# Optimization experiments

Hardware: AMD Instinct MI355X
Metric: run time of the kernel (lower is better)

## Reference

```python
import jax, jax.numpy as jnp
import numpy as np

NB, NX, NU, NY, NQ = 8192, 512, 128, 128, 256


def setup_inputs() -> dict:
    key = jax.random.key(0)
    ks = jax.random.split(key, 13)
    x = jax.random.normal(ks[0], (NB, NX), dtype=jnp.float32)
    u = jax.random.normal(ks[1], (NB, NU), dtype=jnp.float32)
    C1 = jax.random.normal(ks[2], (NQ, NX), dtype=jnp.float32) / np.sqrt(NX).astype(np.float32)
    D11 = jax.random.normal(ks[3], (NQ, NQ), dtype=jnp.float32) / np.sqrt(NQ).astype(np.float32)
    D12 = jax.random.normal(ks[4], (NQ, NU), dtype=jnp.float32) / np.sqrt(NU).astype(np.float32)
    # Lambda is a positive-diagonal matrix (only Lambda[k,k] is used in the recurrence)
    lam_diag = jax.random.uniform(ks[5], (NQ,), dtype=jnp.float32, minval=0.5, maxval=1.5)
    Lambda = jnp.diag(lam_diag)
    bv = 0.1 * jax.random.normal(ks[6], (NQ, 1), dtype=jnp.float32)
    # E must be invertible (set by the REN wrapper in the original code)
    E = jnp.eye(NX, dtype=jnp.float32) + 0.05 * jax.random.normal(ks[7], (NX, NX), dtype=jnp.float32) / np.sqrt(NX).astype(np.float32)
    F = jax.random.normal(ks[8], (NX, NX), dtype=jnp.float32) / np.sqrt(NX).astype(np.float32)
    B1 = jax.random.normal(ks[9], (NX, NQ), dtype=jnp.float32) / np.sqrt(NQ).astype(np.float32)
    B2 = jax.random.normal(ks[10], (NX, NU), dtype=jnp.float32) / np.sqrt(NU).astype(np.float32)
    C2 = jax.random.normal(ks[11], (NY, NX), dtype=jnp.float32) / np.sqrt(NX).astype(np.float32)
    D21 = jax.random.normal(ks[12], (NY, NQ), dtype=jnp.float32) / np.sqrt(NQ).astype(np.float32)
    return {"x": x, "u": u, "C1": C1, "D11": D11, "D12": D12, "Lambda": Lambda,
            "bv": bv, "E": E, "F": F, "B1": B1, "B2": B2, "C2": C2, "D21": D21}


def _solve_w(x, u, C1, D11, D12, lam_diag, bv):
    # Loop-invariant part of v_k: x @ C1[k]^T + u @ D12[k]^T + bv[k]
    base = x @ C1.T + u @ D12.T + bv[:, 0][None, :]  # (nb, nq)
    nb = x.shape[0]
    nq = C1.shape[0]

    def step(w, k):
        # w columns >= k are still zero, matching the torch loop semantics
        v = (base[:, k] + w @ D11[k]) / lam_diag[k]  # (nb,)
        w = w.at[:, k].set(jnp.tanh(v))
        return w, None

    w0 = jnp.zeros((nb, nq), dtype=x.dtype)
    w, _ = jax.lax.scan(step, w0, jnp.arange(nq))
    return w


def reference(x, u, C1, D11, D12, Lambda, bv, E, F, B1, B2, C2, D21):
    lam_diag = jnp.diagonal(Lambda)
    w = _solve_w(x, u, C1, D11, D12, lam_diag, bv)
    # E^{-1} @ M computed via solve (same math as torch.inverse(E) @ M)
    EinvF = jnp.linalg.solve(E, F)
    EinvB1 = jnp.linalg.solve(E, B1)
    EinvB2 = jnp.linalg.solve(E, B2)
    dx = x @ EinvF.T + w @ EinvB1.T + u @ EinvB2.T
    y = x @ C2.T + w @ D21.T
    return (dx, y)
```

## Files before the change

### kernel.cpp

```cpp
#include <hip/hip_runtime.h>

typedef unsigned short u16;
typedef unsigned int   u32;
typedef __attribute__((ext_vector_type(8))) __bf16 bf16x8;
typedef __attribute__((ext_vector_type(4))) float  f32x4;
typedef __attribute__((ext_vector_type(4))) u16    u16x4;
typedef __attribute__((ext_vector_type(4))) u32    u32x4;

#define DEV __device__ __forceinline__

DEV u16 f2b(float f){ union{float f;u32 u;}a; a.f=f; u32 r=a.u + 0x7FFFu + ((a.u>>16)&1u); return (u16)(r>>16); }
DEV float b2f(u16 h){ union{u32 u;float f;}a; a.u=((u32)h)<<16; return a.f; }

typedef __attribute__((address_space(1))) void* gp1;
typedef __attribute__((address_space(3))) void* lp3;
DEV void gl16(const void* g, void* l){
  __builtin_amdgcn_global_load_lds((gp1)g, (lp3)l, 16, 0, 0);
}

__global__ __launch_bounds__(256) void k_prepc(
    const float* __restrict__ x,  const float* __restrict__ u,
    const float* __restrict__ C1, const float* __restrict__ D11,
    const float* __restrict__ D12, const float* __restrict__ Lam,
    const float* __restrict__ E,  const float* __restrict__ F,
    const float* __restrict__ B1, const float* __restrict__ B2,
    const float* __restrict__ C2, const float* __restrict__ D21,
    u16* Ebf, u16* Y0, u16* Z0, u16* McatT, u16* Qt, u16* Rt,
    float* invLam, u16* Ddg2, float* Dt16, u16* P)
{
  if (blockIdx.x < 704) {
    __shared__ float t[32][33];
    int bid = blockIdx.x;
    const int tx = threadIdx.x & 31, ty = threadIdx.x >> 5;
    const float* src; u16* dst; int srcC, nA, task;
    if (bid < 256)      { task = 0; src = E;   srcC = 512; dst = Z0;    nA = 16; }
    else if (bid < 512) { task = 1; src = F;   srcC = 512; dst = McatT; nA = 16; bid -= 256; }
    else if (bid < 640) { task = 2; src = B1;  srcC = 256; dst = McatT + (size_t)640 * 512; nA = 8;  bid -= 512; }
    else                { task = 3; src = B2;  srcC = 128; dst = McatT + (size_t)512 * 512; nA = 4;  bid -= 640; }
    const int a0 = (bid % nA) * 32;
    const int b0 = (bid / nA) * 32;
    #pragma unroll
    for (int k = 0; k < 4; k++) {
      int srow = b0 + ty + 8 * k;
      t[ty + 8 * k][tx] = src[(size_t)srow * srcC + a0 + tx];
    }
    __syncthreads();
    #pragma unroll
    for (int k = 0; k < 4; k++) {
      int drow = a0 + ty + 8 * k, dcol = b0 + tx;
      float v = t[tx][ty + 8 * k];
      if (task == 0) v = ((drow == dcol) ? 2.f : 0.f) - v;
      dst[(size_t)drow * 512 + dcol] = f2b(v);
    }
    return;
  }
  int idx = (blockIdx.x - 704) * 256 + threadIdx.x;
  if (idx < 262144) {
    int i = idx >> 9, j = idx & 511;
    float e = E[idx];
    Ebf[idx] = f2b(e);
    float dij = (i == j) ? 2.f : 0.f;
    Y0[idx] = f2b(dij - e);
    return;
  }
  idx -= 262144;
  if (idx < 114688) {
    int j = idx / 896, k = idx - j * 896;
    float v = (k < 512) ? C2[j * 512 + k]
              : (k < 640 ? 0.f : D21[j * 256 + (k - 640)]);
    Qt[(size_t)(512 + j) * 896 + k] = f2b(v);
    return;
  }
  idx -= 114688;
  if (idx < 163840) {
    int n = idx / 640, k = idx - n * 640;
    float v = (k < 512) ? C1[n * 512 + k] : D12[n * 128 + (k - 512)];
    Rt[idx] = f2b(v);
    return;
  }
  idx -= 163840;
  if (idx < 256) { invLam[idx] = 1.f / Lam[idx * 257]; return; }
  idx -= 256;
  if (idx < 65536) {
    int sb = idx >> 13, t = (idx >> 9) & 15, l = (idx >> 3) & 63, j = idx & 7;
    int r = l & 15, g = l >> 4;
    int n = t * 16 + r, k = sb * 32 + g * 8 + j;
    Ddg2[idx] = f2b(D11[n * 256 + k] * (1.f / Lam[n * 257]));
    return;
  }
  idx -= 65536;
  if (idx < 4096) {
    int T = idx >> 8, k2 = (idx >> 4) & 15, n2 = idx & 15;
    float v = 0.f;
    if (n2 > k2) {
      int n = T * 16 + n2;
      v = D11[n * 256 + T * 16 + k2] * (1.f / Lam[n * 257]);
    }
    Dt16[idx] = v;
    return;
  }
  idx -= 4096;
  {
    int b = idx / 160, t = idx - b * 160;
    f32x4 s; u16* dst;
    if (t < 128) { s = *(const f32x4*)(x + (size_t)b * 512 + t * 4); dst = P + (size_t)b * 896 + t * 4; }
    else         { s = *(const f32x4*)(u + (size_t)b * 128 + (t - 128) * 4); dst = P + (size_t)b * 896 + 512 + (t - 128) * 4; }
    u16x4 o; o.x = f2b(s.x); o.y = f2b(s.y); o.z = f2b(s.z); o.w = f2b(s.w);
    *(u16x4*)dst = o;
  }
}

struct GemmArgs {
  const u16* A; const u16* B; int K; int lda; int ldb;
  u16* outB; int ldB;
  u16* outBT;
  const u16* Yprev;
};

__global__ __launch_bounds__(256) void gemm_b2(
    const u16* __restrict__ A, const u16* __restrict__ B, float* __restrict__ outF,
    const float* __restrict__ bv, const float* __restrict__ iLam)
{
  __shared__ __align__(16) u16 As[64 * 32];
  __shared__ __align__(16) u16 Bs[128 * 32];
  const int bid = blockIdx.x;
  const int wg = (bid & 7) * 32 + (bid >> 3);
  const int bm = wg >> 1, bn = wg & 1;
  const int tid = threadIdx.x;
  const int l = tid & 63, w = tid >> 6;
  const size_t rowbA = 896 * 2, rowbB = 640 * 2;
  const char* Ab = (const char*)A + (size_t)bm * 64 * rowbA;
  const char* Bb = (const char*)B + (size_t)bn * 128 * rowbB;
  const int o = tid * 16, o2 = o + 4096;
  const int rA = o >> 6;
  const int csA = (((o >> 4) ^ rA) & 3) << 4;
  const int rB2 = o2 >> 6;
  const int csB2 = (((o2 >> 4) ^ rB2) & 3) << 4;
  char* AsB = (char*)As; char* BsB = (char*)Bs;
  const int wm = w >> 1, wn = w & 1;
  const int lr = l & 15, lk = l >> 4;
  const int slot = ((lk ^ lr) & 3) << 4;

  f32x4 acc[2][4];
  const f32x4 zz = {0.f, 0.f, 0.f, 0.f};
  #pragma unroll
  for (int i = 0; i < 2; i++)
    #pragma unroll
    for (int j = 0; j < 4; j++) acc[i][j] = zz;

  for (int k0 = 0; k0 < 640; k0 += 32) {
    gl16(Ab + (size_t)rA * rowbA + k0 * 2 + csA, AsB + o);
    gl16(Bb + (size_t)rA * rowbB + k0 * 2 + csA, BsB + o);
    gl16(Bb + (size_t)rB2 * rowbB + k0 * 2 + csB2, BsB + o2);
    __syncthreads();
    bf16x8 af[2], bfv[4];
    #pragma unroll
    for (int mi = 0; mi < 2; mi++)
      af[mi] = *(const bf16x8*)(AsB + (wm * 32 + mi * 16 + lr) * 64 + slot);
    #pragma unroll
    for (int ni = 0; ni < 4; ni++)
      bfv[ni] = *(const bf16x8*)(BsB + (wn * 64 + ni * 16 + lr) * 64 + slot);
    #pragma unroll
    for (int mi = 0; mi < 2; mi++)
      #pragma unroll
      for (int ni = 0; ni < 4; ni++)
        acc[mi][ni] = __builtin_amdgcn_mfma_f32_16x16x32_bf16(af[mi], bfv[ni], acc[mi][ni], 0, 0, 0);
    __syncthreads();
  }

  #pragma unroll
  for (int mi = 0; mi < 2; mi++) {
    #pragma unroll
    for (int ni = 0; ni < 4; ni++) {
      const int row0 = bm * 64 + wm * 32 + mi * 16 + lk * 4;
      const int col  = bn * 128 + wn * 64 + ni * 16 + lr;
      const float bvc = bv[col], il = iLam[col];
      #pragma unroll
      for (int r = 0; r < 4; r++)
        outF[(size_t)(row0 + r) * 256 + col] = (acc[mi][ni][r] + bvc) * il;
    }
  }
}

__global__ __launch_bounds__(256) void gemm_f(
    const u16* __restrict__ A, const u16* __restrict__ B,
    float* __restrict__ dxOut, float* __restrict__ yOut)
{
  __shared__ __align__(16) u16 As[128 * 32];
  __shared__ __align__(16) u16 Bs[64 * 32];
  const int bid = blockIdx.x;
  const int wg = (bid & 7) * 80 + (bid >> 3);
  const int bm = wg / 10, bn = wg - bm * 10;
  const int tid = threadIdx.x;
  const int l = tid & 63, w = tid >> 6;
  const size_t rowb = 896 * 2;
  const char* Ab = (const char*)A + (size_t)bm * 128 * rowb;
  const char* Bb = (const char*)B + (size_t)bn * 64 * rowb;
  const int o = tid * 16, o2 = o + 4096;
  const int r1 = o >> 6, r2 = o2 >> 6;
  const int c1 = (((o >> 4) ^ r1) & 3) << 4;
  const int c2 = (((o2 >> 4) ^ r2) & 3) << 4;
  char* AsB = (char*)As; char* BsB = (char*)Bs;
  const int wm = w >> 1, wn = w & 1;
  const int lr = l & 15, lk = l >> 4;
  const int slot = ((lk ^ lr) & 3) << 4;

  f32x4 acc[4][2];
  const f32x4 zz = {0.f, 0.f, 0.f, 0.f};
  #pragma unroll
  for (int i = 0; i < 4; i++)
    #pragma unroll
    for (int j = 0; j < 2; j++) acc[i][j] = zz;

  for (int k0 = 0; k0 < 896; k0 += 32) {
    gl16(Ab + (size_t)r1 * rowb + k0 * 2 + c1, AsB + o);
    gl16(Ab + (size_t)r2 * rowb + k0 * 2 + c2, AsB + o2);
    gl16(Bb + (size_t)r1 * rowb + k0 * 2 + c1, BsB + o);
    __syncthreads();
    bf16x8 af[4], bfv[2];
    #pragma unroll
    for (int mi = 0; mi < 4; mi++)
      af[mi] = *(const bf16x8*)(AsB + (wm * 64 + mi * 16 + lr) * 64 + slot);
    #pragma unroll
    for (int ni = 0; ni < 2; ni++)
      bfv[ni] = *(const bf16x8*)(BsB + (wn * 32 + ni * 16 + lr) * 64 + slot);
    #pragma unroll
    for (int mi = 0; mi < 4; mi++)
      #pragma unroll
      for (int ni = 0; ni < 2; ni++)
        acc[mi][ni] = __builtin_amdgcn_mfma_f32_16x16x32_bf16(af[mi], bfv[ni], acc[mi][ni], 0, 0, 0);
    __syncthreads();
  }

  #pragma unroll
  for (int mi = 0; mi < 4; mi++) {
    #pragma unroll
    for (int ni = 0; ni < 2; ni++) {
      const int row0 = bm * 128 + wm * 64 + mi * 16 + lk * 4;
      const int col  = bn * 64 + wn * 32 + ni * 16 + lr;
      #pragma unroll
      for (int r = 0; r < 4; r++) {
        float v = acc[mi][ni][r];
        if (col < 512) dxOut[(size_t)(row0 + r) * 512 + col] = v;
        else           yOut[(size_t)(row0 + r) * 128 + (col - 512)] = v;
      }
    }
  }
}

template<int EPI>
DEV void gemm64_body(const GemmArgs& g, int bm, int bn, u16* As, u16* Bs)
{
  const int tid = threadIdx.x;
  const int l = tid & 63, w = tid >> 6;
  const int K = g.K;
  const size_t rowbA = (size_t)g.lda * 2, rowbB = (size_t)g.ldb * 2;
  const char* Ab = (const char*)g.A + (size_t)bm * 64 * rowbA;
  const char* Bb = (const char*)g.B + (size_t)bn * 64 * rowbB;
  const int o = tid * 16;
  const int r0 = o >> 6;
  const int cs = (((o >> 4) ^ r0) & 3) << 4;
  char* AsB = (char*)As; char* BsB = (char*)Bs;
  const int wm = w >> 1, wn = w & 1;
  const int lr = l & 15, lk = l >> 4;
  const int slot = ((lk ^ lr) & 3) << 4;

  f32x4 acc[2][2];
  const f32x4 zz = {0.f, 0.f, 0.f, 0.f};
  acc[0][0] = zz; acc[0][1] = zz; acc[1][0] = zz; acc[1][1] = zz;

  for (int k0 = 0; k0 < K; k0 += 32) {
    gl16(Ab + (size_t)r0 * rowbA + k0 * 2 + cs, AsB + o);
    gl16(Bb + (size_t)r0 * rowbB + k0 * 2 + cs, BsB + o);
    __syncthreads();
    bf16x8 af[2], bfv[2];
    #pragma unroll
    for (int mi = 0; mi < 2; mi++)
      af[mi] = *(const bf16x8*)(AsB + (wm * 32 + mi * 16 + lr) * 64 + slot);
    #pragma unroll
    for (int ni = 0; ni < 2; ni++)
      bfv[ni] = *(const bf16x8*)(BsB + (wn * 32 + ni * 16 + lr) * 64 + slot);
    #pragma unroll
    for (int mi = 0; mi < 2; mi++)
      #pragma unroll
      for (int ni = 0; ni < 2; ni++)
        acc[mi][ni] = __builtin_amdgcn_mfma_f32_16x16x32_bf16(af[mi], bfv[ni], acc[mi][ni], 0, 0, 0);
    __syncthreads();
  }

  #pragma unroll
  for (int mi = 0; mi < 2; mi++) {
    #pragma unroll
    for (int ni = 0; ni < 2; ni++) {
      const int row0 = bm * 64 + wm * 32 + mi * 16 + lk * 4;
      const int col  = bn * 64 + wn * 32 + ni * 16 + lr;
      if (EPI == 2) {
        #pragma unroll
        for (int r = 0; r < 4; r++)
          g.outB[(size_t)(row0 + r) * g.ldB + col] = f2b(acc[mi][ni][r]);
      } else if (EPI == 3) {
        #pragma unroll
        for (int r = 0; r < 4; r++)
          g.outBT[(size_t)col * 512 + (row0 + r)] = f2b(acc[mi][ni][r]);
      } else if (EPI == 4) {
        #pragma unroll
        for (int r = 0; r < 4; r++) {
          int row = row0 + r;
          float d = 2.f * b2f(g.Yprev[row * 512 + col]) - acc[mi][ni][r];
          g.outB[(size_t)row * 512 + col] = f2b(d);
        }
      }
    }
  }
}

template<int EPI>
__global__ __launch_bounds__(256) void gemm64(GemmArgs g)
{
  __shared__ __align__(16) u16 As[64 * 32];
  __shared__ __align__(16) u16 Bs[64 * 32];
  gemm64_body<EPI>(g, blockIdx.y, blockIdx.x, As, Bs);
}

__global__ __launch_bounds__(256) void k_solve_a(
    const float* __restrict__ base2, const u16* __restrict__ Ddg2,
    const float* __restrict__ Dt16, u16* __restrict__ P, GemmArgs ga)
{
  __shared__ __align__(16) char DdL[2][16384];
  __shared__ __align__(16) float DtL[4096];
  __shared__ __align__(16) float tb[4][16][40];

  if (blockIdx.x >= 128) {
    int q = blockIdx.x - 128;
    gemm64_body<3>(ga, q >> 3, q & 7, (u16*)&DdL[0][0], (u16*)&DdL[0][8192]);
    return;
  }

  const int tid = threadIdx.x, l = tid & 63, w = tid >> 6;
  const int r = l & 15, g = l >> 4;
  const int row = blockIdx.x * 64 + w * 16 + r;

  const char* DtG = (const char*)Dt16;
  #pragma unroll
  for (int i = 0; i < 4; i++)
    gl16(DtG + i * 4096 + tid * 16, (char*)DtL + i * 4096 + tid * 16);
  const char* DgG = (const char*)Ddg2;
  #pragma unroll
  for (int i = 0; i < 4; i++)
    gl16(DgG + i * 4096 + tid * 16, DdL[0] + i * 4096 + tid * 16);

  f32x4 st[16];
  const float* bp = base2 + (size_t)row * 256 + g * 4;
  #pragma unroll
  for (int t = 0; t < 16; t++) st[t] = *(const f32x4*)(bp + t * 16);

  u32x4 pkA[8];
  float* tbr = &tb[w][r][0];
  __syncthreads();

  #pragma unroll
  for (int sb = 0; sb < 8; sb++) {
    if (sb < 7) {
      #pragma unroll
      for (int i = 0; i < 4; i++)
        gl16(DgG + (sb + 1) * 16384 + i * 4096 + tid * 16,
             DdL[(sb + 1) & 1] + i * 4096 + tid * 16);
    }
    float ws[8];
    #pragma unroll
    for (int i = 0; i < 8; i++) ws[i] = 0.f;
    f32x4 vv[4];

    *(f32x4*)(tbr + g * 4) = st[2 * sb];
    vv[0] = *(const f32x4*)(tbr);      vv[1] = *(const f32x4*)(tbr + 4);
    vv[2] = *(const f32x4*)(tbr + 8);  vv[3] = *(const f32x4*)(tbr + 12);
    {
      const float* dt = DtL + (2 * sb) * 256;
      #pragma unroll
      for (int k2 = 0; k2 < 16; k2++) {
        float v = vv[k2 >> 2][k2 & 3];
        float ex = __expf(2.f * v);
        float wv = 1.f - 2.f * __fdividef(1.f, ex + 1.f);
        if (g == (k2 >> 3)) ws[k2 & 7] = wv;
        #pragma unroll
        for (int j = k2 >> 2; j < 4; j++)
          vv[j] += wv * *(const f32x4*)(dt + k2 * 16 + j * 4);
      }
    }
    {
      u32x4 pk;
      pk.x = (u32)f2b(ws[0]) | ((u32)f2b(ws[1]) << 16);
      pk.y = (u32)f2b(ws[2]) | ((u32)f2b(ws[3]) << 16);
      pk.z = (u32)f2b(ws[4]) | ((u32)f2b(ws[5]) << 16);
      pk.w = (u32)f2b(ws[6]) | ((u32)f2b(ws[7]) << 16);
      union { u32x4 uu; bf16x8 bb; } cv; cv.uu = pk;
      bf16x8 Af = *(const bf16x8*)(DdL[sb & 1] + (2 * sb + 1) * 1024 + l * 16);
      st[2 * sb + 1] = __builtin_amdgcn_mfma_f32_16x16x32_bf16(Af, cv.bb, st[2 * sb + 1], 0, 0, 0);
    }
    *(f32x4*)(tbr + g * 4) = st[2 * sb + 1];
    vv[0] = *(const f32x4*)(tbr);      vv[1] = *(const f32x4*)(tbr + 4);
    vv[2] = *(const f32x4*)(tbr + 8);  vv[3] = *(const f32x4*)(tbr + 12);
    {
      const float* dt = DtL + (2 * sb + 1) * 256;
      #pragma unroll
      for (int k2 = 0; k2 < 16; k2++) {
        float v = vv[k2 >> 2][k2 & 3];
        float ex = __expf(2.f * v);
        float wv = 1.f - 2.f * __fdividef(1.f, ex + 1.f);
        if (g == 2 + (k2 >> 3)) ws[k2 & 7] = wv;
        #pragma unroll
        for (int j = k2 >> 2; j < 4; j++)
          vv[j] += wv * *(const f32x4*)(dt + k2 * 16 + j * 4);
      }
    }
    {
      u32x4 pk;
      pk.x = (u32)f2b(ws[0]) | ((u32)f2b(ws[1]) << 16);
      pk.y = (u32)f2b(ws[2]) | ((u32)f2b(ws[3]) << 16);
      pk.z = (u32)f2b(ws[4]) | ((u32)f2b(ws[5]) << 16);
      pk.w = (u32)f2b(ws[6]) | ((u32)f2b(ws[7]) << 16);
      pkA[sb] = pk;
      union { u32x4 uu; bf16x8 bb; } cv; cv.uu = pk;
      #pragma unroll
      for (int t = 0; t < 16; t++) {
        if (t >= 2 * sb + 2) {
          bf16x8 Af = *(const bf16x8*)(DdL[sb & 1] + t * 1024 + l * 16);
          st[t] = __builtin_amdgcn_mfma_f32_16x16x32_bf16(Af, cv.bb, st[t], 0, 0, 0);
        }
      }
    }
    __syncthreads();
  }

  u16* Pr = P + (size_t)row * 896 + 640;
  #pragma unroll
  for (int sb = 0; sb < 8; sb++)
    *(u32x4*)(Pr + sb * 32 + g * 8) = pkA[sb];
}

extern "C" void kernel_launch(void* const* d_in, const int* in_sizes, int n_in,
                              void* d_out, int out_size, void* d_ws, size_t ws_size,
                              hipStream_t stream)
{
  const float* x   = (const float*)d_in[0];
  const float* u   = (const float*)d_in[1];
  const float* C1  = (const float*)d_in[2];
  const float* D11 = (const float*)d_in[3];
  const float* D12 = (const float*)d_in[4];
  const float* Lam = (const float*)d_in[5];
  const float* bv  = (const float*)d_in[6];
  const float* E   = (const float*)d_in[7];
  const float* F   = (const float*)d_in[8];
  const float* B1  = (const float*)d_in[9];
  const float* B2  = (const float*)d_in[10];
  const float* C2  = (const float*)d_in[11];
  const float* D21 = (const float*)d_in[12];

  char* ws = (char*)d_ws;
  u16*   P      = (u16*)(ws);
  u16*   Qt     = (u16*)(ws + 14680064);
  u16*   Rt     = (u16*)(ws + 15826944);
  float* base2  = (float*)(ws + 16285696);
  u16*   Ddg2   = (u16*)(ws + 24674304);
  float* Dt16   = (float*)(ws + 24805376);
  u16*   Ebf    = (u16*)(ws + 24838144);
  u16*   Y0     = (u16*)(ws + 25362432);
  u16*   Z0     = (u16*)(ws + 25886720);
  u16*   T0T    = (u16*)(ws + 26411008);
  u16*   Y1     = (u16*)(ws + 26935296);
  u16*   McatT  = (u16*)(ws + 27459584);
  float* invLam = (float*)(ws + 28377088);

  float* dxOut = (float*)d_out;
  float* yOut  = dxOut + (size_t)8192 * 512;

  k_prepc<<<8209, 256, 0, stream>>>(x, u, C1, D11, D12, Lam, E, F, B1, B2, C2, D21,
                                    Ebf, Y0, Z0, McatT, Qt, Rt, invLam, Ddg2, Dt16, P);

  gemm_b2<<<256, 256, 0, stream>>>(P, Rt, base2, bv, invLam);

  GemmArgs a{}; a.A = Ebf; a.B = Z0; a.K = 512; a.lda = 512; a.ldb = 512; a.outBT = T0T;
  k_solve_a<<<192, 256, 0, stream>>>(base2, Ddg2, Dt16, P, a);

  GemmArgs b{}; b.A = Y0; b.B = T0T; b.K = 512; b.lda = 512; b.ldb = 512;
  b.outB = Y1; b.ldB = 512; b.Yprev = Y0;
  gemm64<4><<<dim3(8, 8), 256, 0, stream>>>(b);

  GemmArgs qq{}; qq.A = Y1; qq.B = McatT; qq.K = 512; qq.lda = 512; qq.ldb = 512;
  qq.outB = Qt; qq.ldB = 896;
  gemm64<2><<<dim3(14, 8), 256, 0, stream>>>(qq);

  gemm_f<<<640, 256, 0, stream>>>(P, Qt, dxOut, yOut);
  (void)in_sizes; (void)n_in; (void)out_size; (void)ws_size;
}
```

Measured before the change: 98.40 us.

## Fold side GEMMs into base and solve kernels, halve solve block, widen final GEMM tile

The E-inverse Newton GEMM that writes T0T now runs inside the base GEMM launch as extra blocks, and the Y1 update GEMM runs as extra blocks of the solve kernel. This removes a separate launch and overlaps independent work. The solve kernel drops to 128 threads and 32 rows per block, giving 256 solve blocks so the sequential recurrence spreads over more CUs. The final GEMM tile grows from 128x64 to 128x128, which reuses more data per block but launches fewer blocks and holds more accumulator registers per thread.

Result: faster. 83.95 us (-14.7%).

```diff
diff --git a/kernel.cpp b/kernel.cpp
--- a/kernel.cpp
+++ b/kernel.cpp
@@ -117,12 +117,147 @@
   const u16* Yprev;
 };
 
+template<int EPI>
+DEV void gemm64_body(const GemmArgs& g, int bm, int bn, u16* As, u16* Bs)
+{
+  const int tid = threadIdx.x;
+  const int l = tid & 63, w = tid >> 6;
+  const int K = g.K;
+  const size_t rowbA = (size_t)g.lda * 2, rowbB = (size_t)g.ldb * 2;
+  const char* Ab = (const char*)g.A + (size_t)bm * 64 * rowbA;
+  const char* Bb = (const char*)g.B + (size_t)bn * 64 * rowbB;
+  const int o = tid * 16;
+  const int r0 = o >> 6;
+  const int cs = (((o >> 4) ^ r0) & 3) << 4;
+  char* AsB = (char*)As; char* BsB = (char*)Bs;
+  const int wm = w >> 1, wn = w & 1;
+  const int lr = l & 15, lk = l >> 4;
+  const int slot = ((lk ^ lr) & 3) << 4;
+
+  f32x4 acc[2][2];
+  const f32x4 zz = {0.f, 0.f, 0.f, 0.f};
+  acc[0][0] = zz; acc[0][1] = zz; acc[1][0] = zz; acc[1][1] = zz;
+
+  for (int k0 = 0; k0 < K; k0 += 32) {
+    gl16(Ab + (size_t)r0 * rowbA + k0 * 2 + cs, AsB + o);
+    gl16(Bb + (size_t)r0 * rowbB + k0 * 2 + cs, BsB + o);
+    __syncthreads();
+    bf16x8 af[2], bfv[2];
+    #pragma unroll
+    for (int mi = 0; mi < 2; mi++)
+      af[mi] = *(const bf16x8*)(AsB + (wm * 32 + mi * 16 + lr) * 64 + slot);
+    #pragma unroll
+    for (int ni = 0; ni < 2; ni++)
+      bfv[ni] = *(const bf16x8*)(BsB + (wn * 32 + ni * 16 + lr) * 64 + slot);
+    #pragma unroll
+    for (int mi = 0; mi < 2; mi++)
+      #pragma unroll
+      for (int ni = 0; ni < 2; ni++)
+        acc[mi][ni] = __builtin_amdgcn_mfma_f32_16x16x32_bf16(af[mi], bfv[ni], acc[mi][ni], 0, 0, 0);
+    __syncthreads();
+  }
+
+  #pragma unroll
+  for (int mi = 0; mi < 2; mi++) {
+    #pragma unroll
+    for (int ni = 0; ni < 2; ni++) {
+      const int row0 = bm * 64 + wm * 32 + mi * 16 + lk * 4;
+      const int col  = bn * 64 + wn * 32 + ni * 16 + lr;
+      if (EPI == 2) {
+        #pragma unroll
+        for (int r = 0; r < 4; r++)
+          g.outB[(size_t)(row0 + r) * g.ldB + col] = f2b(acc[mi][ni][r]);
+      } else if (EPI == 3) {
+        #pragma unroll
+        for (int r = 0; r < 4; r++)
+          g.outBT[(size_t)col * 512 + (row0 + r)] = f2b(acc[mi][ni][r]);
+      }
+    }
+  }
+}
+
+template<int EPI>
+DEV void gemm64h_body(const GemmArgs& g, int bm, int bn, u16* As, u16* Bs)
+{
+  const int tid = threadIdx.x;
+  const int l = tid & 63, w = tid >> 6;
+  const int K = g.K;
+  const size_t rowbA = (size_t)g.lda * 2, rowbB = (size_t)g.ldb * 2;
+  const char* Ab = (const char*)g.A + (size_t)bm * 64 * rowbA;
+  const char* Bb = (const char*)g.B + (size_t)bn * 64 * rowbB;
+  const int o1 = tid * 16, o2 = o1 + 2048;
+  const int rA1 = o1 >> 6, rA2 = o2 >> 6;
+  const int cs1 = (((o1 >> 4) ^ rA1) & 3) << 4;
+  const int cs2 = (((o2 >> 4) ^ rA2) & 3) << 4;
+  char* AsB = (char*)As; char* BsB = (char*)Bs;
+  const int lr = l & 15, lk = l >> 4;
+  const int slot = ((lk ^ lr) & 3) << 4;
+
+  f32x4 acc[2][4];
+  const f32x4 zz = {0.f, 0.f, 0.f, 0.f};
+  #pragma unroll
+  for (int i = 0; i < 2; i++)
+    #pragma unroll
+    for (int j = 0; j < 4; j++) acc[i][j] = zz;
+
+  for (int k0 = 0; k0 < K; k0 += 32) {
+    gl16(Ab + (size_t)rA1 * rowbA + k0 * 2 + cs1, AsB + o1);
+    gl16(Ab + (size_t)rA2 * rowbA + k0 * 2 + cs2, AsB + o2);
+    gl16(Bb + (size_t)rA1 * rowbB + k0 * 2 + cs1, BsB + o1);
+    gl16(Bb + (size_t)rA2 * rowbB + k0 * 2 + cs2, BsB + o2);
+    __syncthreads();
+    bf16x8 af[2], bfv[4];
+    #pragma unroll
+    for (int mi = 0; mi < 2; mi++)
+      af[mi] = *(const bf16x8*)(AsB + (w * 32 + mi * 16 + lr) * 64 + slot);
+    #pragma unroll
+    for (int ni = 0; ni < 4; ni++)
+      bfv[ni] = *(const bf16x8*)(BsB + (ni * 16 + lr) * 64 + slot);
+    #pragma unroll
+    for (int mi = 0; mi < 2; mi++)
+      #pragma unroll
+      for (int ni = 0; ni < 4; ni++)
+        acc[mi][ni] = __builtin_amdgcn_mfma_f32_16x16x32_bf16(af[mi], bfv[ni], acc[mi][ni], 0, 0, 0);
+    __syncthreads();
+  }
+
+  #pragma unroll
+  for (int mi = 0; mi < 2; mi++) {
+    #pragma unroll
+    for (int ni = 0; ni < 4; ni++) {
+      const int row0 = bm * 64 + w * 32 + mi * 16 + lk * 4;
+      const int col  = bn * 64 + ni * 16 + lr;
+      if (EPI == 4) {
+        #pragma unroll
+        for (int r = 0; r < 4; r++) {
+          int row = row0 + r;
+          float d = 2.f * b2f(g.Yprev[row * 512 + col]) - acc[mi][ni][r];
+          g.outB[(size_t)row * 512 + col] = f2b(d);
+        }
+      }
+    }
+  }
+}
+
+template<int EPI>
+__global__ __launch_bounds__(256) void gemm64(GemmArgs g)
+{
+  __shared__ __align__(16) u16 As[64 * 32];
+  __shared__ __align__(16) u16 Bs[64 * 32];
+  gemm64_body<EPI>(g, blockIdx.y, blockIdx.x, As, Bs);
+}
+
 __global__ __launch_bounds__(256) void gemm_b2(
     const u16* __restrict__ A, const u16* __restrict__ B, float* __restrict__ outF,
-    const float* __restrict__ bv, const float* __restrict__ iLam)
+    const float* __restrict__ bv, const float* __restrict__ iLam, GemmArgs ga)
 {
   __shared__ __align__(16) u16 As[64 * 32];
   __shared__ __align__(16) u16 Bs[128 * 32];
+  if (blockIdx.x >= 256) {
+    int q = blockIdx.x - 256;
+    gemm64_body<3>(ga, q >> 3, q & 7, As, Bs);
+    return;
+  }
   const int bid = blockIdx.x;
   const int wg = (bid & 7) * 32 + (bid >> 3);
   const int bm = wg >> 1, bn = wg & 1;
@@ -187,47 +322,48 @@
     float* __restrict__ dxOut, float* __restrict__ yOut)
 {
   __shared__ __align__(16) u16 As[128 * 32];
-  __shared__ __align__(16) u16 Bs[64 * 32];
+  __shared__ __align__(16) u16 Bs[128 * 32];
   const int bid = blockIdx.x;
-  const int wg = (bid & 7) * 80 + (bid >> 3);
-  const int bm = wg / 10, bn = wg - bm * 10;
+  const int wg = (bid & 7) * 40 + (bid >> 3);
+  const int bm = wg / 5, bn = wg - bm * 5;
   const int tid = threadIdx.x;
   const int l = tid & 63, w = tid >> 6;
   const size_t rowb = 896 * 2;
   const char* Ab = (const char*)A + (size_t)bm * 128 * rowb;
-  const char* Bb = (const char*)B + (size_t)bn * 64 * rowb;
-  const int o = tid * 16, o2 = o + 4096;
-  const int r1 = o >> 6, r2 = o2 >> 6;
-  const int c1 = (((o >> 4) ^ r1) & 3) << 4;
+  const char* Bb = (const char*)B + (size_t)bn * 128 * rowb;
+  const int o1 = tid * 16, o2 = o1 + 4096;
+  const int r1 = o1 >> 6, r2 = o2 >> 6;
+  const int c1 = (((o1 >> 4) ^ r1) & 3) << 4;
   const int c2 = (((o2 >> 4) ^ r2) & 3) << 4;
   char* AsB = (char*)As; char* BsB = (char*)Bs;
   const int wm = w >> 1, wn = w & 1;
   const int lr = l & 15, lk = l >> 4;
   const int slot = ((lk ^ lr) & 3) << 4;
 
-  f32x4 acc[4][2];
+  f32x4 acc[4][4];
   const f32x4 zz = {0.f, 0.f, 0.f, 0.f};
   #pragma unroll
   for (int i = 0; i < 4; i++)
     #pragma unroll
-    for (int j = 0; j < 2; j++) acc[i][j] = zz;
+    for (int j = 0; j < 4; j++) acc[i][j] = zz;
 
   for (int k0 = 0; k0 < 896; k0 += 32) {
-    gl16(Ab + (size_t)r1 * rowb + k0 * 2 + c1, AsB + o);
+    gl16(Ab + (size_t)r1 * rowb + k0 * 2 + c1, AsB + o1);
     gl16(Ab + (size_t)r2 * rowb + k0 * 2 + c2, AsB + o2);
-    gl16(Bb + (size_t)r1 * rowb + k0 * 2 + c1, BsB + o);
-    __syncthreads();
-    bf16x8 af[4], bfv[2];
+    gl16(Bb + (size_t)r1 * rowb + k0 * 2 + c1, BsB + o1);
+    gl16(Bb + (size_t)r2 * rowb + k0 * 2 + c2, BsB + o2);
+    __syncthreads();
+    bf16x8 af[4], bfv[4];
     #pragma unroll
     for (int mi = 0; mi < 4; mi++)
       af[mi] = *(const bf16x8*)(AsB + (wm * 64 + mi * 16 + lr) * 64 + slot);
     #pragma unroll
-    for (int ni = 0; ni < 2; ni++)
-      bfv[ni] = *(const bf16x8*)(BsB + (wn * 32 + ni * 16 + lr) * 64 + slot);
+    for (int ni = 0; ni < 4; ni++)
+      bfv[ni] = *(const bf16x8*)(BsB + (wn * 64 + ni * 16 + lr) * 64 + slot);
     #pragma unroll
     for (int mi = 0; mi < 4; mi++)
       #pragma unroll
-      for (int ni = 0; ni < 2; ni++)
+      for (int ni = 0; ni < 4; ni++)
         acc[mi][ni] = __builtin_amdgcn_mfma_f32_16x16x32_bf16(af[mi], bfv[ni], acc[mi][ni], 0, 0, 0);
     __syncthreads();
   }
@@ -235,9 +371,9 @@
   #pragma unroll
   for (int mi = 0; mi < 4; mi++) {
     #pragma unroll
-    for (int ni = 0; ni < 2; ni++) {
+    for (int ni = 0; ni < 4; ni++) {
       const int row0 = bm * 128 + wm * 64 + mi * 16 + lk * 4;
-      const int col  = bn * 64 + wn * 32 + ni * 16 + lr;
+      const int col  = bn * 128 + wn * 64 + ni * 16 + lr;
       #pragma unroll
       for (int r = 0; r < 4; r++) {
         float v = acc[mi][ni][r];
@@ -248,106 +384,32 @@
   }
 }
 
-template<int EPI>
-DEV void gemm64_body(const GemmArgs& g, int bm, int bn, u16* As, u16* Bs)
-{
-  const int tid = threadIdx.x;
-  const int l = tid & 63, w = tid >> 6;
-  const int K = g.K;
-  const size_t rowbA = (size_t)g.lda * 2, rowbB = (size_t)g.ldb * 2;
-  const char* Ab = (const char*)g.A + (size_t)bm * 64 * rowbA;
-  const char* Bb = (const char*)g.B + (size_t)bn * 64 * rowbB;
-  const int o = tid * 16;
-  const int r0 = o >> 6;
-  const int cs = (((o >> 4) ^ r0) & 3) << 4;
-  char* AsB = (char*)As; char* BsB = (char*)Bs;
-  const int wm = w >> 1, wn = w & 1;
-  const int lr = l & 15, lk = l >> 4;
-  const int slot = ((lk ^ lr) & 3) << 4;
-
-  f32x4 acc[2][2];
-  const f32x4 zz = {0.f, 0.f, 0.f, 0.f};
-  acc[0][0] = zz; acc[0][1] = zz; acc[1][0] = zz; acc[1][1] = zz;
-
-  for (int k0 = 0; k0 < K; k0 += 32) {
-    gl16(Ab + (size_t)r0 * rowbA + k0 * 2 + cs, AsB + o);
-    gl16(Bb + (size_t)r0 * rowbB + k0 * 2 + cs, BsB + o);
-    __syncthreads();
-    bf16x8 af[2], bfv[2];
-    #pragma unroll
-    for (int mi = 0; mi < 2; mi++)
-      af[mi] = *(const bf16x8*)(AsB + (wm * 32 + mi * 16 + lr) * 64 + slot);
-    #pragma unroll
-    for (int ni = 0; ni < 2; ni++)
-      bfv[ni] = *(const bf16x8*)(BsB + (wn * 32 + ni * 16 + lr) * 64 + slot);
-    #pragma unroll
-    for (int mi = 0; mi < 2; mi++)
-      #pragma unroll
-      for (int ni = 0; ni < 2; ni++)
-        acc[mi][ni] = __builtin_amdgcn_mfma_f32_16x16x32_bf16(af[mi], bfv[ni], acc[mi][ni], 0, 0, 0);
-    __syncthreads();
-  }
-
-  #pragma unroll
-  for (int mi = 0; mi < 2; mi++) {
-    #pragma unroll
-    for (int ni = 0; ni < 2; ni++) {
-      const int row0 = bm * 64 + wm * 32 + mi * 16 + lk * 4;
-      const int col  = bn * 64 + wn * 32 + ni * 16 + lr;
-      if (EPI == 2) {
-        #pragma unroll
-        for (int r = 0; r < 4; r++)
-          g.outB[(size_t)(row0 + r) * g.ldB + col] = f2b(acc[mi][ni][r]);
-      } else if (EPI == 3) {
-        #pragma unroll
-        for (int r = 0; r < 4; r++)
-          g.outBT[(size_t)col * 512 + (row0 + r)] = f2b(acc[mi][ni][r]);
-      } else if (EPI == 4) {
-        #pragma unroll
-        for (int r = 0; r < 4; r++) {
-          int row = row0 + r;
-          float d = 2.f * b2f(g.Yprev[row * 512 + col]) - acc[mi][ni][r];
-          g.outB[(size_t)row * 512 + col] = f2b(d);
-        }
-      }
-    }
-  }
-}
-
-template<int EPI>
-__global__ __launch_bounds__(256) void gemm64(GemmArgs g)
-{
-  __shared__ __align__(16) u16 As[64 * 32];
-  __shared__ __align__(16) u16 Bs[64 * 32];
-  gemm64_body<EPI>(g, blockIdx.y, blockIdx.x, As, Bs);
-}
-
-__global__ __launch_bounds__(256) void k_solve_a(
+__global__ __launch_bounds__(128) void k_solve_a(
     const float* __restrict__ base2, const u16* __restrict__ Ddg2,
     const float* __restrict__ Dt16, u16* __restrict__ P, GemmArgs ga)
 {
   __shared__ __align__(16) char DdL[2][16384];
   __shared__ __align__(16) float DtL[4096];
-  __shared__ __align__(16) float tb[4][16][40];
-
-  if (blockIdx.x >= 128) {
-    int q = blockIdx.x - 128;
-    gemm64_body<3>(ga, q >> 3, q & 7, (u16*)&DdL[0][0], (u16*)&DdL[0][8192]);
+  __shared__ __align__(16) float tb[2][16][40];
+
+  if (blockIdx.x >= 256) {
+    int q = blockIdx.x - 256;
+    gemm64h_body<4>(ga, q >> 3, q & 7, (u16*)&DdL[0][0], (u16*)&DdL[0][4096]);
     return;
   }
 
   const int tid = threadIdx.x, l = tid & 63, w = tid >> 6;
   const int r = l & 15, g = l >> 4;
-  const int row = blockIdx.x * 64 + w * 16 + r;
+  const int row = blockIdx.x * 32 + w * 16 + r;
 
   const char* DtG = (const char*)Dt16;
   #pragma unroll
-  for (int i = 0; i < 4; i++)
-    gl16(DtG + i * 4096 + tid * 16, (char*)DtL + i * 4096 + tid * 16);
+  for (int i = 0; i < 8; i++)
+    gl16(DtG + i * 2048 + tid * 16, (char*)DtL + i * 2048 + tid * 16);
   const char* DgG = (const char*)Ddg2;
   #pragma unroll
-  for (int i = 0; i < 4; i++)
-    gl16(DgG + i * 4096 + tid * 16, DdL[0] + i * 4096 + tid * 16);
+  for (int i = 0; i < 8; i++)
+    gl16(DgG + i * 2048 + tid * 16, DdL[0] + i * 2048 + tid * 16);
 
   f32x4 st[16];
   const float* bp = base2 + (size_t)row * 256 + g * 4;
@@ -362,9 +424,9 @@
   for (int sb = 0; sb < 8; sb++) {
     if (sb < 7) {
       #pragma unroll
-      for (int i = 0; i < 4; i++)
-        gl16(DgG + (sb + 1) * 16384 + i * 4096 + tid * 16,
-             DdL[(sb + 1) & 1] + i * 4096 + tid * 16);
+      for (int i = 0; i < 8; i++)
+        gl16(DgG + (sb + 1) * 16384 + i * 2048 + tid * 16,
+             DdL[(sb + 1) & 1] + i * 2048 + tid * 16);
     }
     float ws[8];
     #pragma unroll
@@ -477,19 +539,17 @@
   k_prepc<<<8209, 256, 0, stream>>>(x, u, C1, D11, D12, Lam, E, F, B1, B2, C2, D21,
                                     Ebf, Y0, Z0, McatT, Qt, Rt, invLam, Ddg2, Dt16, P);
 
-  gemm_b2<<<256, 256, 0, stream>>>(P, Rt, base2, bv, invLam);
-
   GemmArgs a{}; a.A = Ebf; a.B = Z0; a.K = 512; a.lda = 512; a.ldb = 512; a.outBT = T0T;
-  k_solve_a<<<192, 256, 0, stream>>>(base2, Ddg2, Dt16, P, a);
+  gemm_b2<<<320, 256, 0, stream>>>(P, Rt, base2, bv, invLam, a);
 
   GemmArgs b{}; b.A = Y0; b.B = T0T; b.K = 512; b.lda = 512; b.ldb = 512;
   b.outB = Y1; b.ldB = 512; b.Yprev = Y0;
-  gemm64<4><<<dim3(8, 8), 256, 0, stream>>>(b);
+  k_solve_a<<<320, 128, 0, stream>>>(base2, Ddg2, Dt16, P, b);
 
   GemmArgs qq{}; qq.A = Y1; qq.B = McatT; qq.K = 512; qq.lda = 512; qq.ldb = 512;
   qq.outB = Qt; qq.ldB = 896;
   gemm64<2><<<dim3(14, 8), 256, 0, stream>>>(qq);
 
-  gemm_f<<<640, 256, 0, stream>>>(P, Qt, dxOut, yOut);
+  gemm_f<<<320, 256, 0, stream>>>(P, Qt, dxOut, yOut);
   (void)in_sizes; (void)n_in; (void)out_size; (void)ws_size;
 }
```
